# Kernel optimization log

Measured on AMD Instinct MI355X. Metric: run time of the kernel, lower is better.

Reference implementation:

```python
import jax, jax.numpy as jnp
import numpy as np

N_HEAD = 16
LN_EPS = 1e-5


def _layernorm(x, g, b):
    m = x.mean(-1, keepdims=True)
    var = x.var(-1, keepdims=True)
    return (x - m) / jnp.sqrt(var + LN_EPS) * g + b


def setup_inputs() -> dict:
    key = jax.random.key(0)
    B, C, D = 4, 1024, 1024
    ks = jax.random.split(key, 8)
    std = 0.02  # trunc-normal-ish init scale
    inp = {
        "q": jax.random.normal(ks[0], (B, C, D), jnp.float32),
        "k": jax.random.normal(ks[1], (B, C, D), jnp.float32),
        "v": jax.random.normal(ks[2], (B, C, D), jnp.float32),
        # LayerNorm params for norm_k / norm_v (norm_q output is discarded in the source)
        "ln_k_g": jnp.ones((D,), jnp.float32), "ln_k_b": jnp.zeros((D,), jnp.float32),
        "ln_v_g": jnp.ones((D,), jnp.float32), "ln_v_b": jnp.zeros((D,), jnp.float32),
        # Linear projections (stored as [in, out]; x @ W + b)
        "Wq": jax.random.normal(ks[3], (D, D), jnp.float32) * std, "bq": jnp.zeros((D,), jnp.float32),
        "Wk": jax.random.normal(ks[4], (D, D), jnp.float32) * std, "bk": jnp.zeros((D,), jnp.float32),
        "Wv": jax.random.normal(ks[5], (D, D), jnp.float32) * std, "bv": jnp.zeros((D,), jnp.float32),
        "Wo": jax.random.normal(ks[6], (D, D), jnp.float32) * std, "bo": jnp.zeros((D,), jnp.float32),
    }
    return inp


def reference(q, k, v, ln_k_g, ln_k_b, ln_v_g, ln_v_b,
              Wq, bq, Wk, bk, Wv, bv, Wo, bo):
    B, C, D = q.shape
    H = N_HEAD
    Dh = D // H
    scale = Dh ** -0.5

    # Source quirk: q is projected WITHOUT layernorm (norm_q output discarded);
    # k and v are layernormed before projection.
    qp = q @ Wq + bq
    kp = _layernorm(k, ln_k_g, ln_k_b) @ Wk + bk
    vp = _layernorm(v, ln_v_g, ln_v_b) @ Wv + bv

    def split_heads(x):  # [B,C,D] -> [B,H,C,Dh]
        return x.reshape(B, C, H, Dh).transpose(0, 2, 1, 3)

    qh, kh, vh = split_heads(qp), split_heads(kp), split_heads(vp)

    # GELU-activated scores, then scale, then softmax (nonstandard ordering)
    scores = jnp.einsum('bhcd,bhkd->bhck', qh, kh)
    attn = jax.nn.softmax(jax.nn.gelu(scores, approximate=False) * scale, axis=-1)

    out = jnp.einsum('bhck,bhkd->bhcd', attn, vh)  # [B,H,C,Dh]
    out = out.transpose(0, 2, 1, 3).reshape(B, C, D)
    out = out @ Wo + bo
    # F.normalize(dim=-1): L2 normalize with eps clamp
    out = out / jnp.maximum(jnp.linalg.norm(out, axis=-1, keepdims=True), 1e-12)
    # dropout is identity in eval mode
    return out, attn
```

## Files before the change

### kernel.cpp

```cpp
#include <hip/hip_runtime.h>

typedef unsigned short u16;
typedef __attribute__((ext_vector_type(8))) short bf16x8;
typedef __attribute__((ext_vector_type(4))) float f32x4;

__device__ inline float b2f(u16 u) {
  unsigned x = ((unsigned)u) << 16;
  return __uint_as_float(x);
}
__device__ inline u16 f2b(float f) {
  unsigned u = __float_as_uint(f);
  unsigned r = (u + 0x7fffu + ((u >> 16) & 1u)) >> 16;
  return (u16)r;
}

__device__ inline float wsum(float x) {
#pragma unroll
  for (int o = 32; o > 0; o >>= 1) x += __shfl_down(x, o);
  return x;
}

__device__ inline void gl16(const u16* g, u16* l) {
  __builtin_amdgcn_global_load_lds((const __attribute__((address_space(1))) void*)g,
                                   (__attribute__((address_space(3))) void*)l, 16, 0, 0);
}

__global__ __launch_bounds__(256) void prep_kernel(const float* __restrict__ q,
                                                   const float* __restrict__ k,
                                                   const float* __restrict__ v,
                                                   const float* __restrict__ kg,
                                                   const float* __restrict__ kb,
                                                   const float* __restrict__ vg,
                                                   const float* __restrict__ vb,
                                                   u16* __restrict__ QB,
                                                   u16* __restrict__ LNK,
                                                   u16* __restrict__ LNV) {
  __shared__ float red[8];
  int blk = blockIdx.x;
  int mode = blk >> 12;
  long base = (long)(blk & 4095) * 1024;
  int t = threadIdx.x;
  const float* x = mode == 0 ? q : (mode == 1 ? k : v);
  u16* y = mode == 0 ? QB : (mode == 1 ? LNK : LNV);
  float4 raw = *(const float4*)(x + base + t * 4);
  float vv[4] = {raw.x, raw.y, raw.z, raw.w};
  if (mode == 0) {
    u16 o[4];
#pragma unroll
    for (int i = 0; i < 4; i++) o[i] = f2b(vv[i]);
    *(uint2*)(y + base + t * 4) = *(uint2*)o;
    return;
  }
  const float* g = mode == 1 ? kg : vg;
  const float* bb = mode == 1 ? kb : vb;
  float s = 0.f, ss = 0.f;
#pragma unroll
  for (int i = 0; i < 4; i++) { s += vv[i]; ss += vv[i] * vv[i]; }
  s = wsum(s);
  ss = wsum(ss);
  int wid = t >> 6;
  if ((t & 63) == 0) { red[wid] = s; red[4 + wid] = ss; }
  __syncthreads();
  s = red[0] + red[1] + red[2] + red[3];
  ss = red[4] + red[5] + red[6] + red[7];
  float mean = s * (1.f / 1024.f);
  float var = ss * (1.f / 1024.f) - mean * mean;
  float inv = rsqrtf(var + 1e-5f);
  float4 gv = *(const float4*)(g + t * 4);
  float4 bv = *(const float4*)(bb + t * 4);
  float gg[4] = {gv.x, gv.y, gv.z, gv.w};
  float b2[4] = {bv.x, bv.y, bv.z, bv.w};
  u16 outr[4];
#pragma unroll
  for (int i = 0; i < 4; i++) outr[i] = f2b((vv[i] - mean) * inv * gg[i] + b2[i]);
  *(uint2*)(y + base + t * 4) = *(uint2*)outr;
}

__global__ __launch_bounds__(256) void transpose_w4(const float* __restrict__ W0,
                                                    const float* __restrict__ W1,
                                                    const float* __restrict__ W2,
                                                    const float* __restrict__ W3,
                                                    u16* __restrict__ T0, u16* __restrict__ T1,
                                                    u16* __restrict__ T2, u16* __restrict__ T3) {
  int z = blockIdx.z;
  const float* src = z == 0 ? W0 : (z == 1 ? W1 : (z == 2 ? W2 : W3));
  u16* dst = z == 0 ? T0 : (z == 1 ? T1 : (z == 2 ? T2 : T3));
  __shared__ u16 tile[32][33];
  int tx = threadIdx.x & 31, ty = threadIdx.x >> 5;
  int x = blockIdx.x * 32 + tx;
  int y0 = blockIdx.y * 32;
#pragma unroll
  for (int i = 0; i < 32; i += 8) tile[ty + i][tx] = f2b(src[(long)(y0 + ty + i) * 1024 + x]);
  __syncthreads();
  int X = blockIdx.y * 32 + tx;
  int Y0 = blockIdx.x * 32;
#pragma unroll
  for (int i = 0; i < 32; i += 8) dst[(long)(Y0 + ty + i) * 1024 + X] = tile[tx][ty + i];
}

__global__ __launch_bounds__(256) void transpose_v(const u16* __restrict__ vp,
                                                   u16* __restrict__ vT) {
  int z = blockIdx.z;
  const u16* src = vp + (long)(z >> 4) * 1048576 + (long)(z & 15) * 64;
  u16* dst = vT + (long)z * 65536;
  __shared__ u16 tile[32][33];
  int tx = threadIdx.x & 31, ty = threadIdx.x >> 5;
  int c0 = blockIdx.x * 32, d0 = blockIdx.y * 32;
#pragma unroll
  for (int i = 0; i < 32; i += 8) tile[ty + i][tx] = src[(long)(c0 + ty + i) * 1024 + d0 + tx];
  __syncthreads();
#pragma unroll
  for (int i = 0; i < 32; i += 8) dst[(long)(d0 + ty + i) * 1024 + c0 + tx] = tile[tx][ty + i];
}

template <int BM, int BN, typename TC>
__device__ __forceinline__ void gemm_core(const u16* __restrict__ Ab,
                                          const u16* __restrict__ Bb,
                                          const float* __restrict__ bias,
                                          TC* __restrict__ Cb, long m0, long n0) {
  constexpr int TM = BM / 32;
  constexpr int TN = BN / 32;
  __shared__ __align__(16) u16 lsA[BM * 32];
  __shared__ __align__(16) u16 lsB[BN * 32];

  int tid = threadIdx.x;
  int wid = tid >> 6;
  int lane = tid & 63;
  int wm = (wid >> 1) * (BM / 2);
  int wn = (wid & 1) * (BN / 2);
  int lm = lane & 15;
  int quad = lane >> 4;

  f32x4 acc[TM][TN];
#pragma unroll
  for (int i = 0; i < TM; i++)
#pragma unroll
    for (int j = 0; j < TN; j++) acc[i][j] = (f32x4){0.f, 0.f, 0.f, 0.f};

  for (int k0 = 0; k0 < 1024; k0 += 32) {
#pragma unroll
    for (int c = tid; c < BM * 4; c += 256)
      gl16(Ab + (m0 + (c >> 2)) * 1024 + k0 + (c & 3) * 8, &lsA[c * 8]);
#pragma unroll
    for (int c = tid; c < BN * 4; c += 256)
      gl16(Bb + (n0 + (c >> 2)) * 1024 + k0 + (c & 3) * 8, &lsB[c * 8]);
    __syncthreads();
    bf16x8 af[TM], bfr[TN];
#pragma unroll
    for (int i = 0; i < TM; i++)
      af[i] = *(const bf16x8*)&lsA[(wm + i * 16 + lm) * 32 + quad * 8];
#pragma unroll
    for (int j = 0; j < TN; j++)
      bfr[j] = *(const bf16x8*)&lsB[(wn + j * 16 + lm) * 32 + quad * 8];
#pragma unroll
    for (int i = 0; i < TM; i++)
#pragma unroll
      for (int j = 0; j < TN; j++)
        acc[i][j] = __builtin_amdgcn_mfma_f32_16x16x32_bf16(af[i], bfr[j], acc[i][j], 0, 0, 0);
    __syncthreads();
  }

#pragma unroll
  for (int j = 0; j < TN; j++) {
    long n = n0 + wn + j * 16 + lm;
    float bv = bias ? bias[n] : 0.f;
#pragma unroll
    for (int i = 0; i < TM; i++) {
      long mb = m0 + wm + i * 16 + quad * 4;
#pragma unroll
      for (int r = 0; r < 4; r++) {
        float val = acc[i][j][r] + bv;
        if constexpr (sizeof(TC) == 2) Cb[(mb + r) * 1024 + n] = f2b(val);
        else Cb[(mb + r) * 1024 + n] = val;
      }
    }
  }
}

struct QKVArgs {
  const u16* A[3];
  const u16* B[3];
  const float* b[3];
  u16* C[3];
};

__global__ __launch_bounds__(256) void gemm_qkv(QKVArgs g) {
  int z = blockIdx.z;
  gemm_core<128, 128, u16>(g.A[z], g.B[z], g.b[z], g.C[z], (long)blockIdx.x * 128,
                           (long)blockIdx.y * 128);
}

__global__ __launch_bounds__(256) void gemm_o(const u16* __restrict__ A,
                                              const u16* __restrict__ Bt,
                                              const float* __restrict__ bias,
                                              float* __restrict__ C) {
  gemm_core<128, 128, float>(A, Bt, bias, C, (long)blockIdx.x * 128, (long)blockIdx.y * 128);
}

__global__ __launch_bounds__(256) void fused_attn(const u16* __restrict__ QP,
                                                  const u16* __restrict__ KP,
                                                  const u16* __restrict__ VT,
                                                  float* __restrict__ attn,
                                                  u16* __restrict__ CTX) {
  __shared__ __align__(16) u16 P[16 * 1032];
  __shared__ __align__(16) u16 qt[16 * 72];
  __shared__ float wreds[4][16];
  __shared__ float rowinv[16];

  int z = blockIdx.y;
  int b = z >> 4, h = z & 15;
  long q0 = (long)blockIdx.x * 16;
  int tid = threadIdx.x;
  int wid = tid >> 6, lane = tid & 63;
  int lm = lane & 15, quad = lane >> 4;

  const u16* Qb = QP + (long)b * 1048576 + (long)h * 64;
  const u16* Kb = KP + (long)b * 1048576 + (long)h * 64;
  const u16* Vz = VT + (long)z * 65536;
  float* Az = attn + (long)z * 1048576;

  if (tid < 128) {
    int row = tid >> 3, col8 = (tid & 7) * 8;
    *(uint4*)&qt[row * 72 + col8] = *(const uint4*)(Qb + (q0 + row) * 1024 + col8);
  }
  __syncthreads();

  bf16x8 af0 = *(const bf16x8*)&qt[lm * 72 + quad * 8];
  bf16x8 af1 = *(const bf16x8*)&qt[lm * 72 + 32 + quad * 8];

  int ncol0 = wid * 256;
  float sum[4] = {0.f, 0.f, 0.f, 0.f};
#pragma unroll
  for (int jj = 0; jj < 16; jj++) {
    const u16* kr = Kb + (long)(ncol0 + jj * 16 + lm) * 1024;
    bf16x8 bf0 = *(const bf16x8*)(kr + quad * 8);
    bf16x8 bf1 = *(const bf16x8*)(kr + 32 + quad * 8);
    f32x4 s = (f32x4){0.f, 0.f, 0.f, 0.f};
    __builtin_amdgcn_s_setprio(1);
    s = __builtin_amdgcn_mfma_f32_16x16x32_bf16(af0, bf0, s, 0, 0, 0);
    s = __builtin_amdgcn_mfma_f32_16x16x32_bf16(af1, bf1, s, 0, 0, 0);
    __builtin_amdgcn_s_setprio(0);
    int n = ncol0 + jj * 16 + lm;
#pragma unroll
    for (int r = 0; r < 4; r++) {
      float x = s[r];
      float u = 0.70710678118654752f * x;
      float a = fabsf(u);
      float t = __builtin_amdgcn_rcpf(fmaf(0.3275911f, a, 1.0f));
      float p = t * fmaf(t, fmaf(t, fmaf(t, fmaf(t, 1.061405429f, -1.453152027f),
                                         1.421413741f), -0.284496736f), 0.254829592f);
      float eq = __expf(-a * a);
      float erfa = fmaf(-p, eq, 1.0f);
      float erfu = copysignf(erfa, u);
      float hx = 0.0625f * x;
      float logit = fmaf(hx, erfu, hx);
      float e = __expf(logit);
      sum[r] += e;
      P[(quad * 4 + r) * 1032 + n] = f2b(e);
    }
  }

#pragma unroll
  for (int r = 0; r < 4; r++) {
#pragma unroll
    for (int d = 1; d < 16; d <<= 1) sum[r] += __shfl_xor(sum[r], d);
  }
  if (lm == 0) {
#pragma unroll
    for (int r = 0; r < 4; r++) wreds[wid][quad * 4 + r] = sum[r];
  }
  __syncthreads();
  if (tid < 16) rowinv[tid] = 1.f / (wreds[0][tid] + wreds[1][tid] + wreds[2][tid] + wreds[3][tid]);
  __syncthreads();

#pragma unroll
  for (int r = 0; r < 16; r++) {
    float inv = rowinv[r];
    uint2 raw = *(const uint2*)&P[r * 1032 + tid * 4];
    u16* pr = (u16*)&raw;
    f32x4 o;
    o[0] = b2f(pr[0]) * inv;
    o[1] = b2f(pr[1]) * inv;
    o[2] = b2f(pr[2]) * inv;
    o[3] = b2f(pr[3]) * inv;
    __builtin_nontemporal_store(o, (f32x4*)(Az + (q0 + r) * 1024 + tid * 4));
  }

  {
    f32x4 acc = (f32x4){0.f, 0.f, 0.f, 0.f};
    const u16* Vrow = Vz + (long)(wid * 16 + lm) * 1024;
#pragma unroll 4
    for (int kc = 0; kc < 1024; kc += 32) {
      bf16x8 a = *(const bf16x8*)&P[lm * 1032 + kc + quad * 8];
      bf16x8 bv = *(const bf16x8*)(Vrow + kc + quad * 8);
      __builtin_amdgcn_s_setprio(1);
      acc = __builtin_amdgcn_mfma_f32_16x16x32_bf16(a, bv, acc, 0, 0, 0);
      __builtin_amdgcn_s_setprio(0);
    }
    int n = wid * 16 + lm;
    u16* Cb = CTX + (long)b * 1048576 + (long)h * 64;
#pragma unroll
    for (int r = 0; r < 4; r++) {
      float val = acc[r] * rowinv[quad * 4 + r];
      Cb[(q0 + quad * 4 + r) * 1024 + n] = f2b(val);
    }
  }
}

__global__ __launch_bounds__(256) void l2norm_kernel(const float* __restrict__ o,
                                                     float* __restrict__ out) {
  long base = (long)blockIdx.x * 1024;
  int t = threadIdx.x;
  float4 raw = *(const float4*)(o + base + t * 4);
  float v[4] = {raw.x, raw.y, raw.z, raw.w};
  float ss = 0.f;
#pragma unroll
  for (int i = 0; i < 4; i++) ss += v[i] * v[i];
  ss = wsum(ss);
  __shared__ float red[4];
  int wid = t >> 6;
  if ((t & 63) == 0) red[wid] = ss;
  __syncthreads();
  ss = red[0] + red[1] + red[2] + red[3];
  float inv = 1.f / fmaxf(sqrtf(ss), 1e-12f);
  float4 outr = {v[0] * inv, v[1] * inv, v[2] * inv, v[3] * inv};
  *(float4*)(out + base + t * 4) = outr;
}

extern "C" void kernel_launch(void* const* d_in, const int* in_sizes, int n_in,
                              void* d_out, int out_size, void* d_ws, size_t ws_size,
                              hipStream_t stream) {
  const float* q = (const float*)d_in[0];
  const float* k = (const float*)d_in[1];
  const float* v = (const float*)d_in[2];
  const float* ln_k_g = (const float*)d_in[3];
  const float* ln_k_b = (const float*)d_in[4];
  const float* ln_v_g = (const float*)d_in[5];
  const float* ln_v_b = (const float*)d_in[6];
  const float* Wq = (const float*)d_in[7];
  const float* bq = (const float*)d_in[8];
  const float* Wk = (const float*)d_in[9];
  const float* bk = (const float*)d_in[10];
  const float* Wv = (const float*)d_in[11];
  const float* bv_ = (const float*)d_in[12];
  const float* Wo = (const float*)d_in[13];
  const float* bo = (const float*)d_in[14];

  const long MEG = 1024 * 1024;
  u16* ws16 = (u16*)d_ws;
  u16* LNK = ws16;
  u16* LNV = ws16 + 4 * MEG;
  u16* WQT = ws16 + 8 * MEG;
  u16* WKT = ws16 + 9 * MEG;
  u16* WVT = ws16 + 10 * MEG;
  u16* WOT = ws16 + 11 * MEG;
  u16* QP  = ws16 + 12 * MEG;
  u16* KP  = ws16 + 16 * MEG;
  u16* VP  = ws16 + 20 * MEG;
  u16* VT  = ws16 + 24 * MEG;
  u16* QB  = ws16 + 28 * MEG;
  u16* CTX = LNK;
  float* OO = (float*)(ws16 + 12 * MEG);

  float* out = (float*)d_out;
  float* attn = out + 4 * MEG;

  prep_kernel<<<12288, 256, 0, stream>>>(q, k, v, ln_k_g, ln_k_b, ln_v_g, ln_v_b, QB, LNK, LNV);

  transpose_w4<<<dim3(32, 32, 4), 256, 0, stream>>>(Wq, Wk, Wv, Wo, WQT, WKT, WVT, WOT);

  QKVArgs ga;
  ga.A[0] = QB;  ga.A[1] = LNK; ga.A[2] = LNV;
  ga.B[0] = WQT; ga.B[1] = WKT; ga.B[2] = WVT;
  ga.b[0] = bq;  ga.b[1] = bk;  ga.b[2] = bv_;
  ga.C[0] = QP;  ga.C[1] = KP;  ga.C[2] = VP;
  gemm_qkv<<<dim3(32, 8, 3), 256, 0, stream>>>(ga);

  transpose_v<<<dim3(32, 2, 64), 256, 0, stream>>>(VP, VT);

  fused_attn<<<dim3(64, 64), 256, 0, stream>>>(QP, KP, VT, attn, CTX);

  gemm_o<<<dim3(32, 8), 256, 0, stream>>>(CTX, WOT, bo, OO);

  l2norm_kernel<<<4096, 256, 0, stream>>>(OO, out);
}
```

Measured before the change: 520.1 us.

## Fuse V head-transpose into QKV GEMM epilogue and restructure attention softmax/PV

The V projection GEMM now writes its output directly in per-head transposed layout, which removes the separate transpose_v kernel launch and its round trip through global memory. In the attention kernel, QK^T operands are swapped so each lane holds one query row. That allows packed 8-byte stores of P and a cheaper row-sum reduction without the rowinv pass or its extra barrier. The PV loop uses four independent accumulators to break the MFMA dependency chain. The risk is that the transposed epilogue stores are strided 8-byte writes, which could coalesce worse than before.

```diff
diff --git a/kernel.cpp b/kernel.cpp
--- a/kernel.cpp
+++ b/kernel.cpp
@@ -98,22 +98,7 @@
   for (int i = 0; i < 32; i += 8) dst[(long)(Y0 + ty + i) * 1024 + X] = tile[tx][ty + i];
 }
 
-__global__ __launch_bounds__(256) void transpose_v(const u16* __restrict__ vp,
-                                                   u16* __restrict__ vT) {
-  int z = blockIdx.z;
-  const u16* src = vp + (long)(z >> 4) * 1048576 + (long)(z & 15) * 64;
-  u16* dst = vT + (long)z * 65536;
-  __shared__ u16 tile[32][33];
-  int tx = threadIdx.x & 31, ty = threadIdx.x >> 5;
-  int c0 = blockIdx.x * 32, d0 = blockIdx.y * 32;
-#pragma unroll
-  for (int i = 0; i < 32; i += 8) tile[ty + i][tx] = src[(long)(c0 + ty + i) * 1024 + d0 + tx];
-  __syncthreads();
-#pragma unroll
-  for (int i = 0; i < 32; i += 8) dst[(long)(d0 + ty + i) * 1024 + c0 + tx] = tile[tx][ty + i];
-}
-
-template <int BM, int BN, typename TC>
+template <int BM, int BN, typename TC, bool TRANSV>
 __device__ __forceinline__ void gemm_core(const u16* __restrict__ Ab,
                                           const u16* __restrict__ Bb,
                                           const float* __restrict__ bias,
@@ -160,18 +145,37 @@
     __syncthreads();
   }
 
-#pragma unroll
-  for (int j = 0; j < TN; j++) {
-    long n = n0 + wn + j * 16 + lm;
-    float bv = bias ? bias[n] : 0.f;
-#pragma unroll
-    for (int i = 0; i < TM; i++) {
-      long mb = m0 + wm + i * 16 + quad * 4;
-#pragma unroll
-      for (int r = 0; r < 4; r++) {
-        float val = acc[i][j][r] + bv;
-        if constexpr (sizeof(TC) == 2) Cb[(mb + r) * 1024 + n] = f2b(val);
-        else Cb[(mb + r) * 1024 + n] = val;
+  if constexpr (TRANSV) {
+#pragma unroll
+    for (int j = 0; j < TN; j++) {
+      long n = n0 + wn + j * 16 + lm;
+      float bv = bias[n];
+      int h = (int)(n >> 6), dh = (int)(n & 63);
+#pragma unroll
+      for (int i = 0; i < TM; i++) {
+        long mb = m0 + wm + i * 16 + quad * 4;
+        int bidx = (int)(mb >> 10);
+        long c = mb & 1023;
+        u16 pk[4];
+#pragma unroll
+        for (int r = 0; r < 4; r++) pk[r] = f2b(acc[i][j][r] + bv);
+        *(uint2*)((u16*)Cb + ((long)(bidx * 16 + h) * 64 + dh) * 1024 + c) = *(uint2*)pk;
+      }
+    }
+  } else {
+#pragma unroll
+    for (int j = 0; j < TN; j++) {
+      long n = n0 + wn + j * 16 + lm;
+      float bv = bias ? bias[n] : 0.f;
+#pragma unroll
+      for (int i = 0; i < TM; i++) {
+        long mb = m0 + wm + i * 16 + quad * 4;
+#pragma unroll
+        for (int r = 0; r < 4; r++) {
+          float val = acc[i][j][r] + bv;
+          if constexpr (sizeof(TC) == 2) Cb[(mb + r) * 1024 + n] = f2b(val);
+          else Cb[(mb + r) * 1024 + n] = val;
+        }
       }
     }
   }
@@ -186,15 +190,19 @@
 
 __global__ __launch_bounds__(256) void gemm_qkv(QKVArgs g) {
   int z = blockIdx.z;
-  gemm_core<128, 128, u16>(g.A[z], g.B[z], g.b[z], g.C[z], (long)blockIdx.x * 128,
-                           (long)blockIdx.y * 128);
+  long m0 = (long)blockIdx.x * 128, n0 = (long)blockIdx.y * 128;
+  if (z == 2)
+    gemm_core<128, 128, u16, true>(g.A[2], g.B[2], g.b[2], g.C[2], m0, n0);
+  else
+    gemm_core<128, 128, u16, false>(g.A[z], g.B[z], g.b[z], g.C[z], m0, n0);
 }
 
 __global__ __launch_bounds__(256) void gemm_o(const u16* __restrict__ A,
                                               const u16* __restrict__ Bt,
                                               const float* __restrict__ bias,
                                               float* __restrict__ C) {
-  gemm_core<128, 128, float>(A, Bt, bias, C, (long)blockIdx.x * 128, (long)blockIdx.y * 128);
+  gemm_core<128, 128, float, false>(A, Bt, bias, C, (long)blockIdx.x * 128,
+                                    (long)blockIdx.y * 128);
 }
 
 __global__ __launch_bounds__(256) void fused_attn(const u16* __restrict__ QP,
@@ -205,7 +213,6 @@
   __shared__ __align__(16) u16 P[16 * 1032];
   __shared__ __align__(16) u16 qt[16 * 72];
   __shared__ float wreds[4][16];
-  __shared__ float rowinv[16];
 
   int z = blockIdx.y;
   int b = z >> 4, h = z & 15;
@@ -225,22 +232,22 @@
   }
   __syncthreads();
 
-  bf16x8 af0 = *(const bf16x8*)&qt[lm * 72 + quad * 8];
-  bf16x8 af1 = *(const bf16x8*)&qt[lm * 72 + 32 + quad * 8];
+  bf16x8 qf0 = *(const bf16x8*)&qt[lm * 72 + quad * 8];
+  bf16x8 qf1 = *(const bf16x8*)&qt[lm * 72 + 32 + quad * 8];
 
   int ncol0 = wid * 256;
-  float sum[4] = {0.f, 0.f, 0.f, 0.f};
+  float sum = 0.f;
 #pragma unroll
   for (int jj = 0; jj < 16; jj++) {
     const u16* kr = Kb + (long)(ncol0 + jj * 16 + lm) * 1024;
-    bf16x8 bf0 = *(const bf16x8*)(kr + quad * 8);
-    bf16x8 bf1 = *(const bf16x8*)(kr + 32 + quad * 8);
+    bf16x8 kf0 = *(const bf16x8*)(kr + quad * 8);
+    bf16x8 kf1 = *(const bf16x8*)(kr + 32 + quad * 8);
     f32x4 s = (f32x4){0.f, 0.f, 0.f, 0.f};
     __builtin_amdgcn_s_setprio(1);
-    s = __builtin_amdgcn_mfma_f32_16x16x32_bf16(af0, bf0, s, 0, 0, 0);
-    s = __builtin_amdgcn_mfma_f32_16x16x32_bf16(af1, bf1, s, 0, 0, 0);
+    s = __builtin_amdgcn_mfma_f32_16x16x32_bf16(kf0, qf0, s, 0, 0, 0);
+    s = __builtin_amdgcn_mfma_f32_16x16x32_bf16(kf1, qf1, s, 0, 0, 0);
     __builtin_amdgcn_s_setprio(0);
-    int n = ncol0 + jj * 16 + lm;
+    u16 pk[4];
 #pragma unroll
     for (int r = 0; r < 4; r++) {
       float x = s[r];
@@ -255,27 +262,20 @@
       float hx = 0.0625f * x;
       float logit = fmaf(hx, erfu, hx);
       float e = __expf(logit);
-      sum[r] += e;
-      P[(quad * 4 + r) * 1032 + n] = f2b(e);
-    }
-  }
-
-#pragma unroll
-  for (int r = 0; r < 4; r++) {
-#pragma unroll
-    for (int d = 1; d < 16; d <<= 1) sum[r] += __shfl_xor(sum[r], d);
-  }
-  if (lm == 0) {
-#pragma unroll
-    for (int r = 0; r < 4; r++) wreds[wid][quad * 4 + r] = sum[r];
-  }
-  __syncthreads();
-  if (tid < 16) rowinv[tid] = 1.f / (wreds[0][tid] + wreds[1][tid] + wreds[2][tid] + wreds[3][tid]);
+      sum += e;
+      pk[r] = f2b(e);
+    }
+    *(uint2*)&P[lm * 1032 + ncol0 + jj * 16 + quad * 4] = *(uint2*)pk;
+  }
+
+  sum += __shfl_xor(sum, 16);
+  sum += __shfl_xor(sum, 32);
+  if (lane < 16) wreds[wid][lane] = sum;
   __syncthreads();
 
 #pragma unroll
   for (int r = 0; r < 16; r++) {
-    float inv = rowinv[r];
+    float inv = __builtin_amdgcn_rcpf(wreds[0][r] + wreds[1][r] + wreds[2][r] + wreds[3][r]);
     uint2 raw = *(const uint2*)&P[r * 1032 + tid * 4];
     u16* pr = (u16*)&raw;
     f32x4 o;
@@ -287,22 +287,35 @@
   }
 
   {
-    f32x4 acc = (f32x4){0.f, 0.f, 0.f, 0.f};
+    f32x4 a0 = (f32x4){0.f, 0.f, 0.f, 0.f};
+    f32x4 a1 = a0, a2 = a0, a3 = a0;
     const u16* Vrow = Vz + (long)(wid * 16 + lm) * 1024;
-#pragma unroll 4
-    for (int kc = 0; kc < 1024; kc += 32) {
-      bf16x8 a = *(const bf16x8*)&P[lm * 1032 + kc + quad * 8];
-      bf16x8 bv = *(const bf16x8*)(Vrow + kc + quad * 8);
+#pragma unroll 2
+    for (int kc = 0; kc < 1024; kc += 128) {
+      bf16x8 p0 = *(const bf16x8*)&P[lm * 1032 + kc + quad * 8];
+      bf16x8 v0 = *(const bf16x8*)(Vrow + kc + quad * 8);
+      bf16x8 p1 = *(const bf16x8*)&P[lm * 1032 + kc + 32 + quad * 8];
+      bf16x8 v1 = *(const bf16x8*)(Vrow + kc + 32 + quad * 8);
+      bf16x8 p2 = *(const bf16x8*)&P[lm * 1032 + kc + 64 + quad * 8];
+      bf16x8 v2 = *(const bf16x8*)(Vrow + kc + 64 + quad * 8);
+      bf16x8 p3 = *(const bf16x8*)&P[lm * 1032 + kc + 96 + quad * 8];
+      bf16x8 v3 = *(const bf16x8*)(Vrow + kc + 96 + quad * 8);
       __builtin_amdgcn_s_setprio(1);
-      acc = __builtin_amdgcn_mfma_f32_16x16x32_bf16(a, bv, acc, 0, 0, 0);
+      a0 = __builtin_amdgcn_mfma_f32_16x16x32_bf16(p0, v0, a0, 0, 0, 0);
+      a1 = __builtin_amdgcn_mfma_f32_16x16x32_bf16(p1, v1, a1, 0, 0, 0);
+      a2 = __builtin_amdgcn_mfma_f32_16x16x32_bf16(p2, v2, a2, 0, 0, 0);
+      a3 = __builtin_amdgcn_mfma_f32_16x16x32_bf16(p3, v3, a3, 0, 0, 0);
       __builtin_amdgcn_s_setprio(0);
     }
+    f32x4 acc = (a0 + a1) + (a2 + a3);
     int n = wid * 16 + lm;
     u16* Cb = CTX + (long)b * 1048576 + (long)h * 64;
 #pragma unroll
     for (int r = 0; r < 4; r++) {
-      float val = acc[r] * rowinv[quad * 4 + r];
-      Cb[(q0 + quad * 4 + r) * 1024 + n] = f2b(val);
+      int row = quad * 4 + r;
+      float inv = __builtin_amdgcn_rcpf(wreds[0][row] + wreds[1][row] +
+                                        wreds[2][row] + wreds[3][row]);
+      Cb[(q0 + row) * 1024 + n] = f2b(acc[r] * inv);
     }
   }
 }
@@ -356,7 +369,6 @@
   u16* WOT = ws16 + 11 * MEG;
   u16* QP  = ws16 + 12 * MEG;
   u16* KP  = ws16 + 16 * MEG;
-  u16* VP  = ws16 + 20 * MEG;
   u16* VT  = ws16 + 24 * MEG;
   u16* QB  = ws16 + 28 * MEG;
   u16* CTX = LNK;
@@ -373,11 +385,9 @@
   ga.A[0] = QB;  ga.A[1] = LNK; ga.A[2] = LNV;
   ga.B[0] = WQT; ga.B[1] = WKT; ga.B[2] = WVT;
   ga.b[0] = bq;  ga.b[1] = bk;  ga.b[2] = bv_;
-  ga.C[0] = QP;  ga.C[1] = KP;  ga.C[2] = VP;
+  ga.C[0] = QP;  ga.C[1] = KP;  ga.C[2] = VT;
   gemm_qkv<<<dim3(32, 8, 3), 256, 0, stream>>>(ga);
 
-  transpose_v<<<dim3(32, 2, 64), 256, 0, stream>>>(VP, VT);
-
   fused_attn<<<dim3(64, 64), 256, 0, stream>>>(QP, KP, VT, attn, CTX);
 
   gemm_o<<<dim3(32, 8), 256, 0, stream>>>(CTX, WOT, bo, OO);
```

After: 503.3 us. 1.03x faster.
